# Kernel optimization log

Hardware: AMD Instinct MI355X
Metric: run time of the kernel (lower is better)

The kernel has to match this reference:

```python
import jax, jax.numpy as jnp
import numpy as np

CE_W, DICE_W, BD_W = 1.0, 3.0, 2.0   # combined-loss lambdas
BPW = 10.0                            # boundary pixel weight
SMOOTH = 1e-6                         # dice smoothing
# cv2.getStructuringElement(cv2.MORPH_ELLIPSE, (5,5))
ELLIPSE5 = np.array([[0,0,1,0,0],
                     [1,1,1,1,1],
                     [1,1,1,1,1],
                     [1,1,1,1,1],
                     [0,0,1,0,0]], dtype=bool)


def setup_inputs() -> dict:
    key = jax.random.key(0)
    k1, k2 = jax.random.split(key)
    B, C, H, W = 8, 8, 512, 1024
    pred = jax.random.normal(k1, (B, C, H, W), dtype=jnp.float32)
    target = jax.random.randint(k2, (B, H, W), 0, C).astype(jnp.int32)
    return {"pred": pred, "target": target}


def _morph(mask, is_dilate):
    """Grayscale dilate/erode with 5x5 ellipse SE (matches cv2 default border:
    padding value never wins the max/min)."""
    pad_val = 0 if is_dilate else jnp.iinfo(jnp.int32).max
    p = jnp.pad(mask, ((0, 0), (2, 2), (2, 2)), constant_values=pad_val)
    H, W = mask.shape[1], mask.shape[2]
    out = None
    for dy in range(5):
        for dx in range(5):
            if not ELLIPSE5[dy, dx]:
                continue
            s = p[:, dy:dy + H, dx:dx + W]
            if out is None:
                out = s
            else:
                out = jnp.maximum(out, s) if is_dilate else jnp.minimum(out, s)
    return out


def reference(pred, target):
    B, C, H, W = pred.shape
    logp = jax.nn.log_softmax(pred, axis=1)                         # (B,C,H,W)
    # per-pixel cross entropy
    ce_map = -jnp.take_along_axis(logp, target[:, None], axis=1)[:, 0]  # (B,H,W)
    ce = ce_map.mean()
    # dice over softmax probs vs one-hot target
    probs = jnp.exp(logp)
    onehot = jax.nn.one_hot(target, C, dtype=pred.dtype, axis=1)    # (B,C,H,W)
    inter = jnp.sum(probs * onehot, axis=(2, 3))                    # (B,C)
    card = jnp.sum(probs, axis=(2, 3)) + jnp.sum(onehot, axis=(2, 3))
    dice = 1.0 - jnp.mean((2.0 * inter + SMOOTH) / (card + SMOOTH))
    # boundary mask = morphological gradient of the label map
    t = target.astype(jnp.int32)
    boundary = _morph(t, True) - _morph(t, False)                   # (B,H,W)
    wmap = jnp.where(boundary > 0, jnp.float32(BPW), jnp.float32(1.0))
    bd = jnp.mean(ce_map * wmap)
    return CE_W * ce + DICE_W * dice + BD_W * bd
```

## Files before the change

kernel.cpp:

```cpp
#include <hip/hip_runtime.h>
#include <math.h>

constexpr int B = 8, C = 8, H = 512, W = 1024;
constexpr int RH = 2;
constexpr int NT = 256;
constexpr float BPW = 10.0f;
constexpr float SMOOTH = 1e-6f;

constexpr int ACC_N = 2 * B + 3 * B * C;

constexpr int NVALS = 22;
constexpr int PSTRIDE = 24;

__device__ __forceinline__ unsigned win_or5(unsigned lo, unsigned mid, unsigned hi) {
    unsigned long long a = ((unsigned long long)mid << 32) | lo;
    unsigned long long b = ((unsigned long long)hi << 32) | mid;
    return (unsigned)(a >> 16) | (unsigned)(a >> 24) | mid |
           (unsigned)(b >> 8) | (unsigned)(b >> 16);
}

__device__ __forceinline__ unsigned pack_row(const int* __restrict__ tb, int gh, int gc) {
    if (gh < 0 || gh >= H || gc < 0 || gc >= W) return 0u;
    const int4 t4 = *reinterpret_cast<const int4*>(tb + (size_t)gh * W + gc);
    return (1u << t4.x) | ((1u << t4.y) << 8) | ((1u << t4.z) << 16) | ((1u << t4.w) << 24);
}

__global__ __attribute__((amdgpu_waves_per_eu(4, 4))) __launch_bounds__(NT)
void loss_main(const float* __restrict__ pred, const int* __restrict__ target,
               float* __restrict__ acc) {
    __shared__ float sred[32 * PSTRIDE];

    const int tid = threadIdx.x;
    const int lin = blockIdx.x + blockIdx.y * gridDim.x;
    const int swz = (lin & 7) * 256 + (lin >> 3);
    const int h0 = (swz & 255) * RH;
    const int b  = swz >> 8;
    const int gc = tid * 4;

    const int* tb = target + (size_t)b * H * W;
    const size_t plane = (size_t)H * W;
    const float* pb = pred + (size_t)b * C * plane + (size_t)h0 * W + gc;

    float4 xa[C], xb[C];
#pragma unroll
    for (int c = 0; c < C; ++c) xa[c] = *reinterpret_cast<const float4*>(pb + c * plane);
#pragma unroll
    for (int c = 0; c < C; ++c) xb[c] = *reinterpret_cast<const float4*>(pb + c * plane + W);

    const unsigned c0 = pack_row(tb, h0 - 2, gc);
    const unsigned c1 = pack_row(tb, h0 - 1, gc);
    const unsigned c2 = pack_row(tb, h0,     gc);
    const unsigned c3 = pack_row(tb, h0 + 1, gc);
    const unsigned c4 = pack_row(tb, h0 + 2, gc);
    const unsigned c5 = pack_row(tb, h0 + 3, gc);
    const unsigned l0 = pack_row(tb, h0 - 1, gc - 4);
    const unsigned l1 = pack_row(tb, h0,     gc - 4);
    const unsigned l2 = pack_row(tb, h0 + 1, gc - 4);
    const unsigned l3 = pack_row(tb, h0 + 2, gc - 4);
    const unsigned r0 = pack_row(tb, h0 - 1, gc + 4);
    const unsigned r1 = pack_row(tb, h0,     gc + 4);
    const unsigned r2 = pack_row(tb, h0 + 1, gc + 4);
    const unsigned r3 = pack_row(tb, h0 + 2, gc + 4);

    float ce_s = 0.f, bd_s = 0.f;
    float p_s[C], in_s[C];
    unsigned cnt = 0u;
#pragma unroll
    for (int c = 0; c < C; ++c) { p_s[c] = 0.f; in_s[c] = 0.f; }

    const unsigned bmA = win_or5(l0 | l1 | l2, c1 | c2 | c3, r0 | r1 | r2) | c0 | c4;
    const unsigned bmB = win_or5(l1 | l2 | l3, c2 | c3 | c4, r1 | r2 | r3) | c1 | c5;

#pragma unroll
    for (int s = 0; s < 2; ++s) {
        const float4* x = (s == 0) ? xa : xb;
        const unsigned cmid = (s == 0) ? c2 : c3;
        const unsigned bm4  = (s == 0) ? bmA : bmB;

#pragma unroll
        for (int j = 0; j < 4; ++j) {
            const float x0 = (j==0)?x[0].x:(j==1)?x[0].y:(j==2)?x[0].z:x[0].w;
            const float x1 = (j==0)?x[1].x:(j==1)?x[1].y:(j==2)?x[1].z:x[1].w;
            const float x2 = (j==0)?x[2].x:(j==1)?x[2].y:(j==2)?x[2].z:x[2].w;
            const float x3 = (j==0)?x[3].x:(j==1)?x[3].y:(j==2)?x[3].z:x[3].w;
            const float x4 = (j==0)?x[4].x:(j==1)?x[4].y:(j==2)?x[4].z:x[4].w;
            const float x5 = (j==0)?x[5].x:(j==1)?x[5].y:(j==2)?x[5].z:x[5].w;
            const float x6 = (j==0)?x[6].x:(j==1)?x[6].y:(j==2)?x[6].z:x[6].w;
            const float x7 = (j==0)?x[7].x:(j==1)?x[7].y:(j==2)?x[7].z:x[7].w;

            const float e0 = __expf(x0), e1 = __expf(x1), e2 = __expf(x2), e3 = __expf(x3);
            const float e4 = __expf(x4), e5 = __expf(x5), e6 = __expf(x6), e7 = __expf(x7);
            const float sum = ((e0 + e1) + (e2 + e3)) + ((e4 + e5) + (e6 + e7));
            const float invs = __builtin_amdgcn_rcpf(sum);

            const unsigned cm  = (cmid >> (8 * j)) & 0xFFu;
            const unsigned bmj = (bm4  >> (8 * j)) & 0xFFu;
            const int t = 31 - __clz(cm);

            const float p0 = e0 * invs, p1 = e1 * invs, p2 = e2 * invs, p3 = e3 * invs;
            const float p4 = e4 * invs, p5 = e5 * invs, p6 = e6 * invs, p7 = e7 * invs;
            p_s[0] += p0; p_s[1] += p1; p_s[2] += p2; p_s[3] += p3;
            p_s[4] += p4; p_s[5] += p5; p_s[6] += p6; p_s[7] += p7;

            const bool b0 = (t == 0), b1 = (t == 1), b2 = (t == 2), b3 = (t == 3);
            const bool b4 = (t == 4), b5 = (t == 5), b6 = (t == 6), b7 = (t == 7);
            in_s[0] += b0 ? p0 : 0.f;  in_s[1] += b1 ? p1 : 0.f;
            in_s[2] += b2 ? p2 : 0.f;  in_s[3] += b3 ? p3 : 0.f;
            in_s[4] += b4 ? p4 : 0.f;  in_s[5] += b5 ? p5 : 0.f;
            in_s[6] += b6 ? p6 : 0.f;  in_s[7] += b7 ? p7 : 0.f;

            float pt = p0;
            pt = b1 ? p1 : pt;  pt = b2 ? p2 : pt;  pt = b3 ? p3 : pt;
            pt = b4 ? p4 : pt;  pt = b5 ? p5 : pt;  pt = b6 ? p6 : pt;
            pt = b7 ? p7 : pt;
            const float l = __logf(pt);
            const float wgt = (bmj & (bmj - 1u)) ? BPW : 1.f;
            ce_s -= l;
            bd_s = fmaf(-l, wgt, bd_s);
            cnt += 1u << (t << 2);
        }
    }

    float vals[NVALS];
    vals[0] = ce_s; vals[1] = bd_s;
#pragma unroll
    for (int c = 0; c < C; ++c) {
        vals[2 + c]  = p_s[c];
        vals[10 + c] = in_s[c];
    }
#pragma unroll
    for (int q = 0; q < 4; ++q) {
        const float lo = (float)((cnt >> (8 * q)) & 0xFu);
        const float hi = (float)((cnt >> (8 * q + 4)) & 0xFu);
        vals[18 + q] = lo + 4096.f * hi;
    }
#pragma unroll
    for (int k = 0; k < NVALS; ++k) {
        float v = vals[k];
        v += __shfl_down(v, 32, 64);
        v += __shfl_down(v, 16, 64);
        v += __shfl_down(v, 8, 64);
        vals[k] = v;
    }
    const int lane = tid & 63, wid = tid >> 6;
    if (lane < 8) {
        const int p = wid * 8 + lane;
#pragma unroll
        for (int k = 0; k < NVALS; ++k) sred[p * PSTRIDE + k] = vals[k];
    }
    __syncthreads();

    const int k = tid >> 3, j = tid & 7;
    if (k < NVALS) {
        float v = sred[(0 * 8 + j) * PSTRIDE + k] + sred[(1 * 8 + j) * PSTRIDE + k]
                + sred[(2 * 8 + j) * PSTRIDE + k] + sred[(3 * 8 + j) * PSTRIDE + k];
        v += __shfl_down(v, 4, 64);
        v += __shfl_down(v, 2, 64);
        v += __shfl_down(v, 1, 64);
        if (j == 0) {
            if (k == 0)      atomicAdd(&acc[b], v);
            else if (k == 1) atomicAdd(&acc[B + b], v);
            else if (k < 10) atomicAdd(&acc[2 * B + b * C + (k - 2)], v);
            else if (k < 18) atomicAdd(&acc[2 * B + B * C + b * C + (k - 10)], v);
            else {
                const int q = k - 18;
                const float hi = floorf(v * (1.f / 4096.f));
                const float lo = v - 4096.f * hi;
                atomicAdd(&acc[2 * B + 2 * B * C + b * C + 2 * q],     lo);
                atomicAdd(&acc[2 * B + 2 * B * C + b * C + 2 * q + 1], hi);
            }
        }
    }
}

__global__ void loss_final(const float* __restrict__ acc, float* __restrict__ out) {
    const int i = threadIdx.x;
    const float psum  = acc[2 * B + i];
    const float inter = acc[2 * B + B * C + i];
    const float cnt   = acc[2 * B + 2 * B * C + i];
    float d = (2.f * inter + SMOOTH) / (psum + cnt + SMOOTH);
    float ce = (i < B) ? acc[i] : 0.f;
    float bd = (i < B) ? acc[B + i] : 0.f;
#pragma unroll
    for (int off = 32; off > 0; off >>= 1) d += __shfl_down(d, off, 64);
#pragma unroll
    for (int off = 4; off > 0; off >>= 1) {
        ce += __shfl_down(ce, off, 64);
        bd += __shfl_down(bd, off, 64);
    }
    if (i == 0) {
        const float N = (float)B * H * W;
        const float dice = 1.f - d / (float)(B * C);
        out[0] = 1.0f * (ce / N) + 3.0f * dice + 2.0f * (bd / N);
    }
}

extern "C" void kernel_launch(void* const* d_in, const int* in_sizes, int n_in,
                              void* d_out, int out_size, void* d_ws, size_t ws_size,
                              hipStream_t stream) {
    const float* pred = (const float*)d_in[0];
    const int* target = (const int*)d_in[1];
    float* acc = (float*)d_ws;
    float* out = (float*)d_out;

    hipMemsetAsync(acc, 0, ACC_N * sizeof(float), stream);

    dim3 grid(H / RH, B);
    loss_main<<<grid, NT, 0, stream>>>(pred, target, acc);
    loss_final<<<1, 64, 0, stream>>>(acc, out);
}
```

Before: 241.0 us.

## Stage pred tiles into LDS via global_load_lds instead of register loads

Each wave now copies its slice of the RH×C prediction rows into a 64 KB shared buffer using direct global-to-LDS loads, waits on vmcnt, and then reads float4 vectors back from LDS for the softmax/CE math. The aim is to free the VGPRs that held the 16 float4 pred values and let the loads go out asynchronously while the target bitmasks are computed. The waves_per_eu hint is also dropped. In exchange the large LDS allocation limits how many blocks fit per CU, and the extra LDS round trip adds latency.

Result: faster. 224.7 us (-6.8%).

```diff
diff --git a/kernel.cpp b/kernel.cpp
--- a/kernel.cpp
+++ b/kernel.cpp
@@ -12,6 +12,15 @@
 constexpr int NVALS = 22;
 constexpr int PSTRIDE = 24;
 
+typedef float f32x4 __attribute__((ext_vector_type(4)));
+
+__device__ __forceinline__ void gl_lds16(const float* g, float* l) {
+    __builtin_amdgcn_global_load_lds(
+        (const __attribute__((address_space(1))) void*)g,
+        (__attribute__((address_space(3))) void*)l,
+        16, 0, 0);
+}
+
 __device__ __forceinline__ unsigned win_or5(unsigned lo, unsigned mid, unsigned hi) {
     unsigned long long a = ((unsigned long long)mid << 32) | lo;
     unsigned long long b = ((unsigned long long)hi << 32) | mid;
@@ -25,12 +34,14 @@
     return (1u << t4.x) | ((1u << t4.y) << 8) | ((1u << t4.z) << 16) | ((1u << t4.w) << 24);
 }
 
-__global__ __attribute__((amdgpu_waves_per_eu(4, 4))) __launch_bounds__(NT)
+__global__ __launch_bounds__(NT)
 void loss_main(const float* __restrict__ pred, const int* __restrict__ target,
                float* __restrict__ acc) {
+    __shared__ float lds_pred[RH * C * W];
     __shared__ float sred[32 * PSTRIDE];
 
     const int tid = threadIdx.x;
+    const int lane = tid & 63, wid = tid >> 6;
     const int lin = blockIdx.x + blockIdx.y * gridDim.x;
     const int swz = (lin & 7) * 256 + (lin >> 3);
     const int h0 = (swz & 255) * RH;
@@ -39,13 +50,6 @@
 
     const int* tb = target + (size_t)b * H * W;
     const size_t plane = (size_t)H * W;
-    const float* pb = pred + (size_t)b * C * plane + (size_t)h0 * W + gc;
-
-    float4 xa[C], xb[C];
-#pragma unroll
-    for (int c = 0; c < C; ++c) xa[c] = *reinterpret_cast<const float4*>(pb + c * plane);
-#pragma unroll
-    for (int c = 0; c < C; ++c) xb[c] = *reinterpret_cast<const float4*>(pb + c * plane + W);
 
     const unsigned c0 = pack_row(tb, h0 - 2, gc);
     const unsigned c1 = pack_row(tb, h0 - 1, gc);
@@ -62,18 +66,37 @@
     const unsigned r2 = pack_row(tb, h0 + 1, gc + 4);
     const unsigned r3 = pack_row(tb, h0 + 2, gc + 4);
 
+    const int seg = wid * 256;
+#pragma unroll
+    for (int s = 0; s < RH; ++s)
+#pragma unroll
+        for (int c = 0; c < C; ++c) {
+            const float* g = pred + ((size_t)(b * C + c)) * plane
+                                  + (size_t)(h0 + s) * W + seg + lane * 4;
+            float* l = &lds_pred[(s * C + c) * W + seg];
+            gl_lds16(g, l);
+        }
+
+    const unsigned bmA = win_or5(l0 | l1 | l2, c1 | c2 | c3, r0 | r1 | r2) | c0 | c4;
+    const unsigned bmB = win_or5(l1 | l2 | l3, c2 | c3 | c4, r1 | r2 | r3) | c1 | c5;
+
+    __builtin_amdgcn_sched_barrier(0);
+    asm volatile("s_waitcnt vmcnt(0)" ::: "memory");
+    __builtin_amdgcn_sched_barrier(0);
+
     float ce_s = 0.f, bd_s = 0.f;
     float p_s[C], in_s[C];
     unsigned cnt = 0u;
 #pragma unroll
     for (int c = 0; c < C; ++c) { p_s[c] = 0.f; in_s[c] = 0.f; }
 
-    const unsigned bmA = win_or5(l0 | l1 | l2, c1 | c2 | c3, r0 | r1 | r2) | c0 | c4;
-    const unsigned bmB = win_or5(l1 | l2 | l3, c2 | c3 | c4, r1 | r2 | r3) | c1 | c5;
-
-#pragma unroll
-    for (int s = 0; s < 2; ++s) {
-        const float4* x = (s == 0) ? xa : xb;
+#pragma unroll
+    for (int s = 0; s < RH; ++s) {
+        f32x4 x[C];
+#pragma unroll
+        for (int c = 0; c < C; ++c)
+            x[c] = *reinterpret_cast<const f32x4*>(&lds_pred[(s * C + c) * W + gc]);
+
         const unsigned cmid = (s == 0) ? c2 : c3;
         const unsigned bm4  = (s == 0) ? bmA : bmB;
 
@@ -142,7 +165,6 @@
         v += __shfl_down(v, 8, 64);
         vals[k] = v;
     }
-    const int lane = tid & 63, wid = tid >> 6;
     if (lane < 8) {
         const int p = wid * 8 + lane;
 #pragma unroll
```
